# Kernel tuning notes

Measured on AMD Instinct MI355X. Metric: run time of the kernel, lower is better.

The kernel has to match this reference:

```python
import jax, jax.numpy as jnp
import numpy as np

H = 128   # hidden_size
E = 300   # embedding_dim
VOC = 32000
B, TP, TC = 8, 160, 160
D2 = 2 * H  # bidirectional feature dim


def gru_dir(x, Wih, Whh, bih, bhh, reverse):
    # x: [B,T,I] -> hidden states [B,T,Hs]; torch GRU gate order (r,z,n)
    Hs = Whh.shape[1]
    xg = jnp.einsum('bti,gi->btg', x, Wih) + bih  # [B,T,3Hs]
    if reverse:
        xg = xg[:, ::-1]
    def step(h, xt):
        gh = h @ Whh.T + bhh
        xr, xz, xn = jnp.split(xt, 3, axis=-1)
        hr, hz, hn = jnp.split(gh, 3, axis=-1)
        r = jax.nn.sigmoid(xr + hr)
        z = jax.nn.sigmoid(xz + hz)
        n = jnp.tanh(xn + r * hn)
        h = (1.0 - z) * n + z * h
        return h, h
    h0 = jnp.zeros((x.shape[0], Hs), x.dtype)
    _, hs = jax.lax.scan(step, h0, jnp.swapaxes(xg, 0, 1))
    hs = jnp.swapaxes(hs, 0, 1)
    if reverse:
        hs = hs[:, ::-1]
    return hs


def bigru(x, Wf, Uf, bif, bhf, Wb, Ub, bib, bhb):
    return jnp.concatenate([
        gru_dir(x, Wf, Uf, bif, bhf, False),
        gru_dir(x, Wb, Ub, bib, bhb, True)], axis=-1)


def setup_inputs() -> dict:
    key = jax.random.key(0)
    ks = iter(jax.random.split(key, 64))
    def rn(shape, s=0.05):
        return jax.random.normal(next(ks), shape, jnp.float32) * s
    inp = {}
    inp['text_a'] = jax.random.randint(next(ks), (B, TP), 0, VOC)
    inp['text_b'] = jax.random.randint(next(ks), (B, TC), 0, VOC)
    inp['emb'] = rn((VOC, E), 0.1)
    for pfx, ins in [('p', E), ('c', E), ('a', 6 * D2)]:
        for d in ('f', 'b'):
            inp[pfx + '_Wih_' + d] = rn((3 * H, ins))
            inp[pfx + '_Whh_' + d] = rn((3 * H, H))
            inp[pfx + '_bih_' + d] = jnp.zeros((3 * H,), jnp.float32)
            inp[pfx + '_bhh_' + d] = jnp.zeros((3 * H,), jnp.float32)
    inp['Wc1'] = rn((H, D2)); inp['Wc2'] = rn((H, D2)); inp['Vc'] = rn((H,))
    inp['Wb'] = rn((D2, D2))
    inp['Wd'] = rn((H, D2)); inp['Vd'] = rn((H,))
    inp['Wm'] = rn((H, D2)); inp['Vm'] = rn((H,))
    inp['Ws'] = rn((H, D2)); inp['Vs'] = rn((H,))
    inp['Wp'] = rn((H, D2)); inp['Vp'] = rn((H,))
    inp['W1'] = rn((H, D2)); inp['W2'] = rn((H, D2)); inp['Vv'] = rn((H,))
    inp['Wout'] = rn((2, D2)); inp['bout'] = jnp.zeros((2,), jnp.float32)
    return inp


def _forward(text_a, text_b, emb,
             p_Wih_f, p_Whh_f, p_bih_f, p_bhh_f, p_Wih_b, p_Whh_b, p_bih_b, p_bhh_b,
             c_Wih_f, c_Whh_f, c_bih_f, c_bhh_f, c_Wih_b, c_Whh_b, c_bih_b, c_bhh_b,
             a_Wih_f, a_Whh_f, a_bih_f, a_bhh_f, a_Wih_b, a_Whh_b, a_bih_b, a_bhh_b,
             Wc1, Wc2, Vc, Wb, Wd, Vd, Wm, Vm, Ws, Vs, Wp, Vp, W1, W2, Vv, Wout, bout):
    hp = bigru(emb[text_a], p_Wih_f, p_Whh_f, p_bih_f, p_bhh_f,
               p_Wih_b, p_Whh_b, p_bih_b, p_bhh_b)          # [B,Tp,2H]
    hc = bigru(emb[text_b], c_Wih_f, c_Whh_f, c_bih_f, c_bhh_f,
               c_Wih_b, c_Whh_b, c_bih_b, c_bhh_b)          # [B,Tc,2H]
    # concat (additive) attention: [B,Tc,Tp,H]
    s = jnp.tanh((hp @ Wc1.T)[:, None] + (hc @ Wc2.T)[:, :, None])
    a_cat = jax.nn.softmax(s @ Vc, axis=2)                   # [B,Tc,Tp]
    concat_rep = jnp.einsum('bct,btd->bcd', a_cat, hp)
    # bilinear attention
    a_bil = jax.nn.softmax(jnp.einsum('bcd,btd->bct', hc, hp @ Wb.T), axis=2)
    bil_rep = jnp.einsum('bct,btd->bcd', a_bil, hp)
    # dot / minus attention on [B,Tc,Tp,2H] broadcasts
    hp4 = hp[:, None]; hc4 = hc[:, :, None]
    a_dot = jax.nn.softmax(jnp.tanh((hp4 * hc4) @ Wd.T) @ Vd, axis=2)
    dot_rep = jnp.einsum('bct,btd->bcd', a_dot, hp)
    a_min = jax.nn.softmax(jnp.tanh((hp4 - hc4) @ Wm.T) @ Vm, axis=2)
    minus_rep = jnp.einsum('bct,btd->bcd', a_min, hp)
    # self attention on hc: [B,Tc,Tc,2H]
    a_self = jax.nn.softmax(jnp.tanh((hc[:, None] * hc[:, :, None]) @ Ws.T) @ Vs, axis=2)
    self_rep = jnp.einsum('bct,btd->bcd', a_self, hc)
    agg_in = jnp.concatenate([hc, self_rep, concat_rep, dot_rep, bil_rep, minus_rep], axis=-1)
    agg = bigru(agg_in, a_Wih_f, a_Whh_f, a_bih_f, a_bhh_f,
                a_Wih_b, a_Whh_b, a_bih_b, a_bhh_b)          # [B,Tc,2H]
    # pooled passage rep
    ap = jax.nn.softmax(jnp.tanh(hp @ Wp.T) @ Vp, axis=-1)   # [B,Tp]
    rp = jnp.einsum('bt,btd->bd', ap, hp)                    # [B,2H]
    # final attention over aggregation (note: no tanh, faithful to source)
    sc = (agg @ W1.T + (rp @ W2.T)[:, None]) @ Vv            # [B,Tc]
    ac = jax.nn.softmax(sc, axis=-1)
    rc = jnp.einsum('bc,bcd->bd', ac, agg)                   # [B,2H]
    return rc @ Wout.T + bout                                # [B,2] logits


def reference(text_a, text_b, emb,
              p_Wih_f, p_Whh_f, p_bih_f, p_bhh_f, p_Wih_b, p_Whh_b, p_bih_b, p_bhh_b,
              c_Wih_f, c_Whh_f, c_bih_f, c_bhh_f, c_Wih_b, c_Whh_b, c_bih_b, c_bhh_b,
              a_Wih_f, a_Whh_f, a_bih_f, a_bhh_f, a_Wih_b, a_Whh_b, a_bih_b, a_bhh_b,
              Wc1, Wc2, Vc, Wb, Wd, Vd, Wm, Vm, Ws, Vs, Wp, Vp, W1, W2, Vv, Wout, bout):
    return _forward(text_a, text_b, emb,
                    p_Wih_f, p_Whh_f, p_bih_f, p_bhh_f, p_Wih_b, p_Whh_b, p_bih_b, p_bhh_b,
                    c_Wih_f, c_Whh_f, c_bih_f, c_bhh_f, c_Wih_b, c_Whh_b, c_bih_b, c_bhh_b,
                    a_Wih_f, a_Whh_f, a_bih_f, a_bhh_f, a_Wih_b, a_Whh_b, a_bih_b, a_bhh_b,
                    Wc1, Wc2, Vc, Wb, Wd, Vd, Wm, Vm, Ws, Vs, Wp, Vp, W1, W2, Vv, Wout, bout)
```

## Files before the change

### kernel.cpp

```cpp
#include <hip/hip_runtime.h>

#define BB 8
#define TT 160
#define EE 300
#define HH 128
#define D2 256
#define G3 384
#define PSTR 40

typedef __attribute__((ext_vector_type(8))) short bf16x8;
typedef __attribute__((ext_vector_type(4))) float floatx4;

__device__ inline float fsigmoid(float x){ return 1.f/(1.f+__expf(-x)); }
__device__ inline float ftanh(float x){ return 2.f*fsigmoid(2.f*x) - 1.f; }

__device__ inline void split2(float x, unsigned short& hi, unsigned short& lo){
  unsigned ux = __float_as_uint(x);
  hi = (unsigned short)(ux>>16);
  float r = x - __uint_as_float(ux & 0xFFFF0000u);
  lo = (unsigned short)(__float_as_uint(r)>>16);
}

__global__ __launch_bounds__(256) void k_embed(const int* ta, const int* tb,
    const float* emb, float* ep, float* ec){
  const int idx = blockIdx.x*256 + threadIdx.x;
  const int per = BB*TT*EE;
  if (idx < per){
    const int e = idx % EE, bt = idx / EE;
    ep[idx] = emb[(long)ta[bt]*EE + e];
  } else {
    const int j = idx - per;
    const int e = j % EE, bt = j / EE;
    ec[j] = emb[(long)tb[bt]*EE + e];
  }
}

__global__ __launch_bounds__(256) void k_splitarr(const float* a, const float* b, int n,
    unsigned short* ahi, unsigned short* alo, unsigned short* bhi, unsigned short* blo){
  const int idx = blockIdx.x*256 + threadIdx.x;
  if (idx < n){
    split2(a[idx], ahi[idx], alo[idx]);
    split2(b[idx], bhi[idx], blo[idx]);
  }
}

struct GemmJob {
  const float* A; const float* W; const float* bias;
  float* C; int N; int K;
};
struct GemmJobs { GemmJob j[6]; };

__global__ __launch_bounds__(256) void k_gemm(GemmJobs jobs){
  const GemmJob J = jobs.j[blockIdx.z];
  const int tid = threadIdx.x;
  const int lane = tid & 63, w = tid >> 6;
  const int l15 = lane & 15, q = lane >> 4;
  const int n0 = blockIdx.x * 64;
  if (n0 >= J.N) return;
  const int K = J.K;
  const long mrow = blockIdx.y*64 + w*16 + l15;
  const float* Arow = J.A + mrow*K;
  floatx4 acc[4];
  #pragma unroll
  for (int t=0;t<4;t++) acc[t] = (floatx4)0.f;
  const int nch = (K+31)>>5;
  for (int kc=0; kc<nch; kc++){
    const int k0 = kc<<5;
    const int kb = k0 + q*8;
    const bool full = (k0+32 <= K);
    float av[8];
    if (full){
      const floatx4 a0 = *(const floatx4*)(Arow+kb);
      const floatx4 a1 = *(const floatx4*)(Arow+kb+4);
      av[0]=a0[0];av[1]=a0[1];av[2]=a0[2];av[3]=a0[3];
      av[4]=a1[0];av[5]=a1[1];av[6]=a1[2];av[7]=a1[3];
    } else {
      #pragma unroll
      for (int j=0;j<8;j++){ const int k=kb+j; av[j] = (k<K)? Arow[k] : 0.f; }
    }
    union { bf16x8 v; unsigned short u[8]; } ahi, alo;
    #pragma unroll
    for (int j=0;j<8;j++) split2(av[j], ahi.u[j], alo.u[j]);
    #pragma unroll
    for (int t=0;t<4;t++){
      const int n = n0 + t*16 + l15;
      const float* Wr = J.W + (long)n*K + kb;
      float wv[8];
      if (full){
        const floatx4 w0 = *(const floatx4*)(Wr);
        const floatx4 w1 = *(const floatx4*)(Wr+4);
        wv[0]=w0[0];wv[1]=w0[1];wv[2]=w0[2];wv[3]=w0[3];
        wv[4]=w1[0];wv[5]=w1[1];wv[6]=w1[2];wv[7]=w1[3];
      } else {
        #pragma unroll
        for (int j=0;j<8;j++){ const int k=kb+j; wv[j] = (k<K)? Wr[j] : 0.f; }
      }
      union { bf16x8 v; unsigned short u[8]; } whi, wlo;
      #pragma unroll
      for (int j=0;j<8;j++) split2(wv[j], whi.u[j], wlo.u[j]);
      acc[t] = __builtin_amdgcn_mfma_f32_16x16x32_bf16(ahi.v, whi.v, acc[t], 0,0,0);
      acc[t] = __builtin_amdgcn_mfma_f32_16x16x32_bf16(ahi.v, wlo.v, acc[t], 0,0,0);
      acc[t] = __builtin_amdgcn_mfma_f32_16x16x32_bf16(alo.v, whi.v, acc[t], 0,0,0);
    }
  }
  const long rbase = blockIdx.y*64 + w*16 + q*4;
  #pragma unroll
  for (int t=0;t<4;t++){
    const int n = n0 + t*16 + l15;
    const float bv = J.bias ? J.bias[n] : 0.f;
    #pragma unroll
    for (int r=0;r<4;r++)
      J.C[(rbase+r)*(long)J.N + n] = acc[t][r] + bv;
  }
}

struct GruJob { const float* xg; const float* Whh; const float* bhh; float* out; int ocol; int rev; };
struct GruJobs { GruJob j[4]; };

__global__ __launch_bounds__(768) void k_gru(GruJobs jobs){
  const GruJob J = jobs.j[blockIdx.y];
  const int bi = blockIdx.x;
  const int tid = threadIdx.x;
  const int g = tid >> 1, p = tid & 1;
  __shared__ float h_sh[HH];
  __shared__ float gh_sh[G3];
  __shared__ float xt_sh[G3];
  float wr[64];
  {
    const float* wp = J.Whh + (long)g*HH + p*64;
    #pragma unroll
    for (int k=0;k<64;k+=4){
      const floatx4 t4 = *(const floatx4*)(wp+k);
      wr[k]=t4[0]; wr[k+1]=t4[1]; wr[k+2]=t4[2]; wr[k+3]=t4[3];
    }
  }
  const float bhh = J.bhh[g];
  if (tid < HH) h_sh[tid] = 0.f;
  float hreg = 0.f;
  float xv = 0.f;
  {
    const int t0 = J.rev ? (TT-1) : 0;
    if (tid < G3) xv = J.xg[((long)bi*TT + t0)*G3 + tid];
  }
  __syncthreads();
  for (int t=0;t<TT;t++){
    const int tt = J.rev ? (TT-1-t) : t;
    if (tid < G3) xt_sh[tid] = xv;
    if (t+1 < TT){
      const int tn = J.rev ? (TT-2-t) : (t+1);
      if (tid < G3) xv = J.xg[((long)bi*TT + tn)*G3 + tid];
    }
    float gh = 0.f;
    #pragma unroll
    for (int k=0;k<64;k+=4){
      const floatx4 h4 = *(const floatx4*)&h_sh[p*64 + k];
      gh += wr[k]*h4[0] + wr[k+1]*h4[1] + wr[k+2]*h4[2] + wr[k+3]*h4[3];
    }
    gh += __shfl_xor(gh, 1);
    if (p==0) gh_sh[g] = gh + bhh;
    __syncthreads();
    if (tid < HH){
      const float r = fsigmoid(xt_sh[tid]       + gh_sh[tid]);
      const float z = fsigmoid(xt_sh[tid+HH]    + gh_sh[tid+HH]);
      const float n = ftanh  (xt_sh[tid+2*HH]  + r*gh_sh[tid+2*HH]);
      const float h = (1.f-z)*n + z*hreg;
      hreg = h;
      h_sh[tid] = h;
      J.out[((long)bi*TT + tt)*D2 + J.ocol + tid] = h;
    }
    __syncthreads();
  }
}

__device__ inline float block_softmax160(float s, int tid, float* red){
  float m = s;
  #pragma unroll
  for (int o=32;o>0;o>>=1) m = fmaxf(m, __shfl_xor(m,o));
  if ((tid&63)==0) red[tid>>6] = m;
  __syncthreads();
  m = fmaxf(fmaxf(red[0],red[1]), fmaxf(red[2],red[3]));
  const float p = (tid<TT) ? __expf(s-m) : 0.f;
  float t = p;
  #pragma unroll
  for (int o=32;o>0;o>>=1) t += __shfl_xor(t,o);
  if ((tid&63)==0) red[4+(tid>>6)] = t;
  __syncthreads();
  const float sum = red[4]+red[5]+red[6]+red[7];
  return p / sum;
}

__device__ inline float block_softmax160_512(float s, int tid, float* red){
  float m = s;
  #pragma unroll
  for (int o=32;o>0;o>>=1) m = fmaxf(m, __shfl_xor(m,o));
  if ((tid&63)==0) red[tid>>6] = m;
  __syncthreads();
  m = red[0];
  #pragma unroll
  for (int i=1;i<8;i++) m = fmaxf(m, red[i]);
  const float p = (tid<TT) ? __expf(s-m) : 0.f;
  float t = p;
  #pragma unroll
  for (int o=32;o>0;o>>=1) t += __shfl_xor(t,o);
  if ((tid&63)==0) red[8+(tid>>6)] = t;
  __syncthreads();
  float sum = red[8];
  #pragma unroll
  for (int i=1;i<8;i++) sum += red[8+i];
  return p / sum;
}

struct PairJob { const unsigned short* Phi; const unsigned short* Plo;
                 const float* Q; const float* W; const float* V; float* a_out; };

__global__ __launch_bounds__(512) void k_pairattn(PairJob j0, PairJob j1){
  const PairJob J = blockIdx.z ? j1 : j0;
  const int b = blockIdx.y, c = blockIdx.x;
  const int tid = threadIdx.x;
  const int lane = tid & 63, w = tid >> 6;
  const int l15 = lane & 15, q = lane >> 4;
  __shared__ unsigned short Pb[2*2*160*PSTR];
  __shared__ float Qs[D2];
  __shared__ float sc_sh[TT];
  __shared__ float red[16];
  if (tid < D2) Qs[tid] = J.Q[((long)b*TT + c)*D2 + tid];
  if (tid < TT) sc_sh[tid] = 0.f;
  const long pbase = (long)b*TT*D2;

  int s_hl[5], s_t[5], s_d4[5];
  #pragma unroll
  for (int r=0;r<5;r++){
    const int idx = tid + r*512;
    const int hl = (idx >= 1280) ? 1 : 0;
    const int e4 = idx - hl*1280;
    s_hl[r] = hl; s_t[r] = e4 >> 3; s_d4[r] = e4 & 7;
  }
  uint2 stg[5];
  #pragma unroll
  for (int r=0;r<5;r++){
    const unsigned short* src = (s_hl[r] ? J.Plo : J.Phi) + pbase + (long)s_t[r]*D2 + 0*32 + s_d4[r]*4;
    stg[r] = *(const uint2*)src;
  }
  const float* Wbase = J.W + (long)(w*16 + l15)*D2;
  floatx4 wv0 = *(const floatx4*)(Wbase + q*8);
  floatx4 wv1 = *(const floatx4*)(Wbase + q*8 + 4);
  #pragma unroll
  for (int r=0;r<5;r++)
    *(uint2*)&Pb[((0*2 + s_hl[r])*160 + s_t[r])*PSTR + s_d4[r]*4] = stg[r];
  __syncthreads();

  floatx4 acc[10];
  #pragma unroll
  for (int nt=0;nt<10;nt++) acc[nt] = (floatx4)0.f;

  for (int kc=0; kc<8; kc++){
    const floatx4 wc0 = wv0, wc1 = wv1;
    if (kc < 7){
      wv0 = *(const floatx4*)(Wbase + (kc+1)*32 + q*8);
      wv1 = *(const floatx4*)(Wbase + (kc+1)*32 + q*8 + 4);
      #pragma unroll
      for (int r=0;r<5;r++){
        const unsigned short* src = (s_hl[r] ? J.Plo : J.Phi) + pbase + (long)s_t[r]*D2 + (kc+1)*32 + s_d4[r]*4;
        stg[r] = *(const uint2*)src;
      }
    }
    const int d0 = kc*32 + q*8;
    const floatx4 q0 = *(const floatx4*)&Qs[d0];
    const floatx4 q1 = *(const floatx4*)&Qs[d0+4];
    union { bf16x8 v; unsigned short u[8]; } ah, al;
    #pragma unroll
    for (int j=0;j<4;j++){
      split2(wc0[j]*q0[j], ah.u[j],   al.u[j]);
      split2(wc1[j]*q1[j], ah.u[4+j], al.u[4+j]);
    }
    const int buf = kc & 1;
    #pragma unroll
    for (int nt=0;nt<10;nt++){
      const int t = nt*16 + l15;
      union { bf16x8 v; } bh, bl;
      bh.v = *(const bf16x8*)&Pb[((buf*2+0)*160 + t)*PSTR + q*8];
      bl.v = *(const bf16x8*)&Pb[((buf*2+1)*160 + t)*PSTR + q*8];
      acc[nt] = __builtin_amdgcn_mfma_f32_16x16x32_bf16(ah.v, bh.v, acc[nt], 0,0,0);
      acc[nt] = __builtin_amdgcn_mfma_f32_16x16x32_bf16(ah.v, bl.v, acc[nt], 0,0,0);
      acc[nt] = __builtin_amdgcn_mfma_f32_16x16x32_bf16(al.v, bh.v, acc[nt], 0,0,0);
    }
    if (kc < 7){
      const int nbuf = 1 - buf;
      #pragma unroll
      for (int r=0;r<5;r++)
        *(uint2*)&Pb[((nbuf*2 + s_hl[r])*160 + s_t[r])*PSTR + s_d4[r]*4] = stg[r];
      __syncthreads();
    }
  }

  float vreg[4];
  #pragma unroll
  for (int r=0;r<4;r++) vreg[r] = J.V[w*16 + q*4 + r];
  #pragma unroll
  for (int nt=0;nt<10;nt++){
    float pp = 0.f;
    #pragma unroll
    for (int r=0;r<4;r++) pp += vreg[r]*ftanh(acc[nt][r]);
    pp += __shfl_xor(pp,16);
    pp += __shfl_xor(pp,32);
    if (q==0) atomicAdd(&sc_sh[nt*16 + l15], pp);
  }
  __syncthreads();
  const float s = (tid<TT)? sc_sh[tid] : -INFINITY;
  const float a = block_softmax160_512(s, tid, red);
  if (tid < TT) J.a_out[((long)b*TT + c)*TT + tid] = a;
}

struct AddJob { const float* up; const float* uc; const float* V; float sgn; float* a_out; };

__global__ __launch_bounds__(256) void k_addattn(AddJob j0, AddJob j1){
  const AddJob J = blockIdx.z ? j1 : j0;
  const int b = blockIdx.y, c = blockIdx.x, tid = threadIdx.x;
  __shared__ float ucc[HH];
  __shared__ float vv[HH];
  __shared__ float red[8];
  if (tid < HH){
    ucc[tid] = J.sgn * J.uc[((long)b*TT + c)*HH + tid];
    vv[tid] = J.V[tid];
  }
  __syncthreads();
  float s = -INFINITY;
  if (tid < TT){
    const float* ur = J.up + ((long)b*TT + tid)*HH;
    float a0 = 0.f;
    #pragma unroll 4
    for (int k=0;k<HH;k++) a0 += vv[k]*ftanh(ur[k]+ucc[k]);
    s = a0;
  }
  const float a = block_softmax160(s, tid, red);
  if (tid < TT) J.a_out[((long)b*TT + c)*TT + tid] = a;
}

__global__ __launch_bounds__(256) void k_bilattn(const float* hc, const float* hpWb, float* a_out){
  const int b = blockIdx.y, c = blockIdx.x, tid = threadIdx.x;
  __shared__ float hcc[D2];
  __shared__ float red[8];
  if (tid < D2) hcc[tid] = hc[((long)b*TT + c)*D2 + tid];
  __syncthreads();
  float s = -INFINITY;
  if (tid < TT){
    const float* pr = hpWb + ((long)b*TT + tid)*D2;
    float a0 = 0.f;
    #pragma unroll 4
    for (int k=0;k<D2;k++) a0 += hcc[k]*pr[k];
    s = a0;
  }
  const float a = block_softmax160(s, tid, red);
  if (tid < TT) a_out[((long)b*TT + c)*TT + tid] = a;
}

__global__ __launch_bounds__(256) void k_rep(const float* hp, const float* hc,
    const float* acat, const float* abil, const float* adot, const float* amin, const float* aself,
    float* aggin){
  const int b = blockIdx.y, c = blockIdx.x, tid = threadIdx.x;
  __shared__ float a5[5][TT];
  {
    const long base = ((long)b*TT + c)*TT;
    for (int i=tid;i<5*TT;i+=256){
      const int which = i/TT, t = i - which*TT;
      const float* p = which==0? acat : which==1? abil : which==2? adot : which==3? amin : aself;
      a5[which][t] = p[base + t];
    }
  }
  __syncthreads();
  const float* hpb = hp + (long)b*TT*D2 + tid;
  const float* hcb = hc + (long)b*TT*D2 + tid;
  float r0=0.f,r1=0.f,r2=0.f,r3=0.f,r4=0.f;
  for (int t=0;t<TT;t++){
    const float vp = hpb[(long)t*D2];
    const float vc = hcb[(long)t*D2];
    r0 += a5[0][t]*vp;
    r1 += a5[1][t]*vp;
    r2 += a5[2][t]*vp;
    r3 += a5[3][t]*vp;
    r4 += a5[4][t]*vc;
  }
  float* o = aggin + ((long)b*TT + c)*(6*D2);
  o[tid]        = hc[((long)b*TT + c)*D2 + tid];
  o[D2 + tid]   = r4;
  o[2*D2 + tid] = r0;
  o[3*D2 + tid] = r2;
  o[4*D2 + tid] = r1;
  o[5*D2 + tid] = r3;
}

__global__ __launch_bounds__(256) void k_tail1(const float* upP, const float* Vp,
    const float* hp, float* rp){
  const int b = blockIdx.x, tid = threadIdx.x;
  __shared__ float vv[HH];
  __shared__ float ap_sh[TT];
  __shared__ float red[8];
  if (tid<HH) vv[tid] = Vp[tid];
  __syncthreads();
  float s = -INFINITY;
  if (tid<TT){
    const float* ur = upP + ((long)b*TT + tid)*HH;
    float a0=0.f;
    #pragma unroll 4
    for (int k=0;k<HH;k++) a0 += vv[k]*ftanh(ur[k]);
    s = a0;
  }
  const float a = block_softmax160(s, tid, red);
  if (tid<TT) ap_sh[tid] = a;
  __syncthreads();
  float acc = 0.f;
  const float* hpb = hp + (long)b*TT*D2 + tid;
  for (int t=0;t<TT;t++) acc += ap_sh[t]*hpb[(long)t*D2];
  rp[b*D2 + tid] = acc;
}

__global__ __launch_bounds__(256) void k_tail2(const float* aggW1, const float* agg, const float* rp,
    const float* W2, const float* Vv, const float* Wout, const float* bout,
    float* out){
  const int b = blockIdx.x, tid = threadIdx.x;
  __shared__ float rpw[HH];
  __shared__ float ac_sh[TT];
  __shared__ float rc_sh[D2];
  __shared__ float red[8];
  if (tid < HH){
    float a0=0.f;
    const float* wr2 = W2 + (long)tid*D2;
    const float* rr = rp + b*D2;
    for (int d=0; d<D2; d++) a0 += wr2[d]*rr[d];
    rpw[tid] = a0;
  }
  __syncthreads();
  float s = -INFINITY;
  if (tid < TT){
    const float* ar = aggW1 + ((long)b*TT + tid)*HH;
    float a0=0.f;
    for (int k=0;k<HH;k++) a0 += Vv[k]*(ar[k] + rpw[k]);
    s = a0;
  }
  const float a = block_softmax160(s, tid, red);
  if (tid < TT) ac_sh[tid] = a;
  __syncthreads();
  float rc=0.f;
  const float* ab = agg + (long)b*TT*D2 + tid;
  for (int t=0;t<TT;t++) rc += ac_sh[t]*ab[(long)t*D2];
  rc_sh[tid] = rc;
  __syncthreads();
  if (tid < 2){
    float o = bout[tid];
    const float* wr = Wout + (long)tid*D2;
    for (int d=0; d<D2; d++) o += wr[d]*rc_sh[d];
    out[b*2 + tid] = o;
  }
}

extern "C" void kernel_launch(void* const* d_in, const int* in_sizes, int n_in,
                              void* d_out, int out_size, void* d_ws, size_t ws_size,
                              hipStream_t stream){
  (void)in_sizes; (void)n_in; (void)out_size; (void)ws_size;
  const int* ta = (const int*)d_in[0];
  const int* tb = (const int*)d_in[1];
  const float* emb = (const float*)d_in[2];
  #define F32(i) ((const float*)d_in[i])

  float* ws = (float*)d_ws;
  float* ep    = ws;
  float* ec    = ep    + 384000;
  float* xg_pf = ec    + 384000;
  float* xg_pb = xg_pf + 491520;
  float* xg_cf = xg_pb + 491520;
  float* xg_cb = xg_cf + 491520;
  float* hp    = xg_cb + 491520;
  float* hc    = hp    + 327680;
  float* up1   = hc    + 327680;
  float* uc2   = up1   + 163840;
  float* ump   = uc2   + 163840;
  float* umc   = ump   + 163840;
  float* upP   = umc   + 163840;
  float* hpWb  = upP   + 163840;
  float* acat  = hpWb  + 327680;
  float* abil  = acat  + 204800;
  float* adot  = abil  + 204800;
  float* amin  = adot  + 204800;
  float* aself = amin  + 204800;
  float* aggin = aself + 204800;
  float* rp    = aggin + 1966080;
  unsigned short* hp_hi = (unsigned short*)(rp + 2048);
  unsigned short* hp_lo = hp_hi + 327680;
  unsigned short* hc_hi = hp_lo + 327680;
  unsigned short* hc_lo = hc_hi + 327680;
  float* xg_af = xg_pf;
  float* xg_ab = xg_pb;
  float* agg   = xg_cf;
  float* aggW1 = xg_cb;

  k_embed<<<dim3(3000), dim3(256), 0, stream>>>(ta, tb, emb, ep, ec);

  GemmJobs ja = {};
  ja.j[0] = {ep, F32(3),  F32(5),  xg_pf, 384, 300};
  ja.j[1] = {ep, F32(7),  F32(9),  xg_pb, 384, 300};
  ja.j[2] = {ec, F32(11), F32(13), xg_cf, 384, 300};
  ja.j[3] = {ec, F32(15), F32(17), xg_cb, 384, 300};
  k_gemm<<<dim3(6,20,4), dim3(256), 0, stream>>>(ja);

  GruJobs gj = {};
  gj.j[0] = {xg_pf, F32(4),  F32(6),  hp, 0,   0};
  gj.j[1] = {xg_pb, F32(8),  F32(10), hp, 128, 1};
  gj.j[2] = {xg_cf, F32(12), F32(14), hc, 0,   0};
  gj.j[3] = {xg_cb, F32(16), F32(18), hc, 128, 1};
  k_gru<<<dim3(8,4), dim3(768), 0, stream>>>(gj);

  k_splitarr<<<dim3(1280), dim3(256), 0, stream>>>(hp, hc, 327680, hp_hi, hp_lo, hc_hi, hc_lo);

  GemmJobs jb = {};
  jb.j[0] = {hp, F32(27), nullptr, up1,  128, 256};
  jb.j[1] = {hc, F32(28), nullptr, uc2,  128, 256};
  jb.j[2] = {hp, F32(33), nullptr, ump,  128, 256};
  jb.j[3] = {hc, F32(33), nullptr, umc,  128, 256};
  jb.j[4] = {hp, F32(37), nullptr, upP,  128, 256};
  jb.j[5] = {hp, F32(30), nullptr, hpWb, 256, 256};
  k_gemm<<<dim3(4,20,6), dim3(256), 0, stream>>>(jb);

  PairJob pd  = {hp_hi, hp_lo, hc, F32(31), F32(32), adot};
  PairJob psf = {hc_hi, hc_lo, hc, F32(35), F32(36), aself};
  k_pairattn<<<dim3(160,8,2), dim3(512), 0, stream>>>(pd, psf);

  AddJob ac_ = {up1, uc2, F32(29),  1.f, acat};
  AddJob am_ = {ump, umc, F32(34), -1.f, amin};
  k_addattn<<<dim3(160,8,2), dim3(256), 0, stream>>>(ac_, am_);

  k_bilattn<<<dim3(160,8), dim3(256), 0, stream>>>(hc, hpWb, abil);

  k_tail1<<<dim3(8), dim3(256), 0, stream>>>(upP, F32(38), hp, rp);

  k_rep<<<dim3(160,8), dim3(256), 0, stream>>>(hp, hc, acat, abil, adot, amin, aself, aggin);

  GemmJobs jc = {};
  jc.j[0] = {aggin, F32(19), F32(21), xg_af, 384, 1536};
  jc.j[1] = {aggin, F32(23), F32(25), xg_ab, 384, 1536};
  k_gemm<<<dim3(6,20,2), dim3(256), 0, stream>>>(jc);

  GruJobs gja = {};
  gja.j[0] = {xg_af, F32(20), F32(22), agg, 0,   0};
  gja.j[1] = {xg_ab, F32(24), F32(26), agg, 128, 1};
  k_gru<<<dim3(8,2), dim3(768), 0, stream>>>(gja);

  GemmJobs jd = {};
  jd.j[0] = {agg, F32(39), nullptr, aggW1, 128, 256};
  k_gemm<<<dim3(2,20,1), dim3(256), 0, stream>>>(jd);

  k_tail2<<<dim3(8), dim3(256), 0, stream>>>(aggW1, agg, rp, F32(40), F32(41), F32(42), F32(43),
                                             (float*)d_out);
  #undef F32
}
```

Before: 927.5 us.

## Compute GRU recurrent matvec with split-bf16 MFMA and double-buffered hidden state

The recurrent h·Whh^T product in the GRU kernel now runs on bf16 MFMA instructions, using a hi/lo split of both weights and hidden state so results stay close to fp32. Weights are pre-split into registers, and 8 waves each own 16 rows of every gate. The hidden state is double-buffered in shared memory, so only one barrier per timestep is needed instead of two. Each gate update now runs in the lanes that own the accumulator rows. The cost is extra MFMA work, since only one column of the 16-wide B operand is used, plus per-step split overhead and a small precision change.

```diff
diff --git a/kernel.cpp b/kernel.cpp
--- a/kernel.cpp
+++ b/kernel.cpp
@@ -117,56 +117,102 @@
 struct GruJob { const float* xg; const float* Whh; const float* bhh; float* out; int ocol; int rev; };
 struct GruJobs { GruJob j[4]; };
 
-__global__ __launch_bounds__(768) void k_gru(GruJobs jobs){
+__global__ __launch_bounds__(512) void k_gru(GruJobs jobs){
   const GruJob J = jobs.j[blockIdx.y];
   const int bi = blockIdx.x;
   const int tid = threadIdx.x;
-  const int g = tid >> 1, p = tid & 1;
-  __shared__ float h_sh[HH];
-  __shared__ float gh_sh[G3];
-  __shared__ float xt_sh[G3];
-  float wr[64];
-  {
-    const float* wp = J.Whh + (long)g*HH + p*64;
-    #pragma unroll
-    for (int k=0;k<64;k+=4){
-      const floatx4 t4 = *(const floatx4*)(wp+k);
-      wr[k]=t4[0]; wr[k+1]=t4[1]; wr[k+2]=t4[2]; wr[k+3]=t4[3];
-    }
-  }
-  const float bhh = J.bhh[g];
-  if (tid < HH) h_sh[tid] = 0.f;
-  float hreg = 0.f;
-  float xv = 0.f;
+  const int lane = tid & 63, w = tid >> 6;
+  const int l15 = lane & 15, q = lane >> 4;
+  const bool act = (l15 == 0);
+  __shared__ float h_sh[2][132];
+
+  union BF { bf16x8 v; unsigned short u[8]; };
+  BF Ah[3][4], Al[3][4];
+  #pragma unroll
+  for (int it=0; it<3; it++){
+    const float* wr = J.Whh + (long)((it*8 + w)*16 + l15)*HH;
+    #pragma unroll
+    for (int kc=0; kc<4; kc++){
+      const floatx4 w0 = *(const floatx4*)(wr + kc*32 + q*8);
+      const floatx4 w1 = *(const floatx4*)(wr + kc*32 + q*8 + 4);
+      #pragma unroll
+      for (int jj=0; jj<4; jj++){
+        split2(w0[jj], Ah[it][kc].u[jj],   Al[it][kc].u[jj]);
+        split2(w1[jj], Ah[it][kc].u[4+jj], Al[it][kc].u[4+jj]);
+      }
+    }
+  }
+  const int j0 = w*16 + q*4;
+  floatx4 bhr = *(const floatx4*)(J.bhh + j0);
+  floatx4 bhz = *(const floatx4*)(J.bhh + 128 + j0);
+  floatx4 bhn = *(const floatx4*)(J.bhh + 256 + j0);
+  floatx4 hreg = (floatx4)0.f;
+
+  for (int i = tid; i < 2*132; i += 512) ((float*)h_sh)[i] = 0.f;
+
+  floatx4 xr=(floatx4)0.f, xz=(floatx4)0.f, xn=(floatx4)0.f;
   {
     const int t0 = J.rev ? (TT-1) : 0;
-    if (tid < G3) xv = J.xg[((long)bi*TT + t0)*G3 + tid];
-  }
-  __syncthreads();
-  for (int t=0;t<TT;t++){
+    if (act){
+      const float* xgp = J.xg + ((long)bi*TT + t0)*G3;
+      xr = *(const floatx4*)(xgp + j0);
+      xz = *(const floatx4*)(xgp + 128 + j0);
+      xn = *(const floatx4*)(xgp + 256 + j0);
+    }
+  }
+  __syncthreads();
+
+  for (int t=0; t<TT; t++){
     const int tt = J.rev ? (TT-1-t) : t;
-    if (tid < G3) xt_sh[tid] = xv;
-    if (t+1 < TT){
+    const int buf = t & 1;
+    const floatx4 cxr=xr, cxz=xz, cxn=xn;
+    if (act && t+1 < TT){
       const int tn = J.rev ? (TT-2-t) : (t+1);
-      if (tid < G3) xv = J.xg[((long)bi*TT + tn)*G3 + tid];
-    }
-    float gh = 0.f;
-    #pragma unroll
-    for (int k=0;k<64;k+=4){
-      const floatx4 h4 = *(const floatx4*)&h_sh[p*64 + k];
-      gh += wr[k]*h4[0] + wr[k+1]*h4[1] + wr[k+2]*h4[2] + wr[k+3]*h4[3];
-    }
-    gh += __shfl_xor(gh, 1);
-    if (p==0) gh_sh[g] = gh + bhh;
-    __syncthreads();
-    if (tid < HH){
-      const float r = fsigmoid(xt_sh[tid]       + gh_sh[tid]);
-      const float z = fsigmoid(xt_sh[tid+HH]    + gh_sh[tid+HH]);
-      const float n = ftanh  (xt_sh[tid+2*HH]  + r*gh_sh[tid+2*HH]);
-      const float h = (1.f-z)*n + z*hreg;
-      hreg = h;
-      h_sh[tid] = h;
-      J.out[((long)bi*TT + tt)*D2 + J.ocol + tid] = h;
+      const float* xgp = J.xg + ((long)bi*TT + tn)*G3;
+      xr = *(const floatx4*)(xgp + j0);
+      xz = *(const floatx4*)(xgp + 128 + j0);
+      xn = *(const floatx4*)(xgp + 256 + j0);
+    }
+    floatx4 accr=(floatx4)0.f, accz=(floatx4)0.f, accn=(floatx4)0.f;
+    #pragma unroll
+    for (int kc=0; kc<4; kc++){
+      BF Bh2, Bl2;
+      if (act){
+        const float* hp8 = &h_sh[buf][kc*32 + q*8];
+        const floatx4 h0 = *(const floatx4*)hp8;
+        const floatx4 h1 = *(const floatx4*)(hp8+4);
+        #pragma unroll
+        for (int jj=0; jj<4; jj++){
+          split2(h0[jj], Bh2.u[jj],   Bl2.u[jj]);
+          split2(h1[jj], Bh2.u[4+jj], Bl2.u[4+jj]);
+        }
+      } else {
+        #pragma unroll
+        for (int jj=0; jj<8; jj++){ Bh2.u[jj]=0; Bl2.u[jj]=0; }
+      }
+      accr = __builtin_amdgcn_mfma_f32_16x16x32_bf16(Ah[0][kc].v, Bh2.v, accr, 0,0,0);
+      accz = __builtin_amdgcn_mfma_f32_16x16x32_bf16(Ah[1][kc].v, Bh2.v, accz, 0,0,0);
+      accn = __builtin_amdgcn_mfma_f32_16x16x32_bf16(Ah[2][kc].v, Bh2.v, accn, 0,0,0);
+      accr = __builtin_amdgcn_mfma_f32_16x16x32_bf16(Ah[0][kc].v, Bl2.v, accr, 0,0,0);
+      accz = __builtin_amdgcn_mfma_f32_16x16x32_bf16(Ah[1][kc].v, Bl2.v, accz, 0,0,0);
+      accn = __builtin_amdgcn_mfma_f32_16x16x32_bf16(Ah[2][kc].v, Bl2.v, accn, 0,0,0);
+      accr = __builtin_amdgcn_mfma_f32_16x16x32_bf16(Al[0][kc].v, Bh2.v, accr, 0,0,0);
+      accz = __builtin_amdgcn_mfma_f32_16x16x32_bf16(Al[1][kc].v, Bh2.v, accz, 0,0,0);
+      accn = __builtin_amdgcn_mfma_f32_16x16x32_bf16(Al[2][kc].v, Bh2.v, accn, 0,0,0);
+    }
+    const int nbuf = 1 - buf;
+    if (act){
+      floatx4 hnew;
+      #pragma unroll
+      for (int r=0; r<4; r++){
+        const float gr = fsigmoid(cxr[r] + accr[r] + bhr[r]);
+        const float gz = fsigmoid(cxz[r] + accz[r] + bhz[r]);
+        const float gn = ftanh  (cxn[r] + gr*(accn[r] + bhn[r]));
+        hnew[r] = (1.f-gz)*gn + gz*hreg[r];
+      }
+      hreg = hnew;
+      *(floatx4*)&h_sh[nbuf][j0] = hnew;
+      *(floatx4*)(J.out + ((long)bi*TT + tt)*D2 + J.ocol + j0) = hnew;
     }
     __syncthreads();
   }
@@ -507,7 +553,7 @@
   gj.j[1] = {xg_pb, F32(8),  F32(10), hp, 128, 1};
   gj.j[2] = {xg_cf, F32(12), F32(14), hc, 0,   0};
   gj.j[3] = {xg_cb, F32(16), F32(18), hc, 128, 1};
-  k_gru<<<dim3(8,4), dim3(768), 0, stream>>>(gj);
+  k_gru<<<dim3(8,4), dim3(512), 0, stream>>>(gj);
 
   k_splitarr<<<dim3(1280), dim3(256), 0, stream>>>(hp, hc, 327680, hp_hi, hp_lo, hc_hi, hc_lo);
 
@@ -542,7 +588,7 @@
   GruJobs gja = {};
   gja.j[0] = {xg_af, F32(20), F32(22), agg, 0,   0};
   gja.j[1] = {xg_ab, F32(24), F32(26), agg, 128, 1};
-  k_gru<<<dim3(8,2), dim3(768), 0, stream>>>(gja);
+  k_gru<<<dim3(8,2), dim3(512), 0, stream>>>(gja);
 
   GemmJobs jd = {};
   jd.j[0] = {agg, F32(39), nullptr, aggW1, 128, 256};
```

New measurement: 1.532 ms. 1.65x slower.

## Pre-split GEMM weights once and shrink GRU block to fuse gate math

Applied to the files above, without the earlier changes.

A new kernel converts every GEMM weight matrix into bf16 hi/lo halves (padded in K) once per call, so the GEMM kernels load the split values instead of re-splitting fp32 weights in every tile. The GRU kernel moves from 768 to 256 threads: each thread pair keeps all three gate rows of Whh in registers, computes the r/z/n dot products together, and applies the gate nonlinearities in the same threads, using a double-buffered hidden state. This removes the gh/xt shared-memory round trip and one barrier per timestep from the serial recurrence. The cost is an extra weight-split launch plus scratch memory, and 192 weight registers per thread in the GRU, which risks spilling.

```diff
diff --git a/kernel.cpp b/kernel.cpp
--- a/kernel.cpp
+++ b/kernel.cpp
@@ -44,20 +44,32 @@
   }
 }
 
-struct GemmJob {
-  const float* A; const float* W; const float* bias;
-  float* C; int N; int K;
+struct SplitJob { const float* W; unsigned short* hi; unsigned short* lo; int n; int K; int Kp; };
+struct SplitJobs { SplitJob j[12]; };
+
+__global__ __launch_bounds__(256) void k_splitw(SplitJobs jobs){
+  const SplitJob J = jobs.j[blockIdx.z];
+  const int idx = blockIdx.x*256 + threadIdx.x;
+  if (idx >= J.n) return;
+  const int row = idx / J.Kp, k = idx - row*J.Kp;
+  const float v = (k < J.K) ? J.W[(long)row*J.K + k] : 0.f;
+  split2(v, J.hi[idx], J.lo[idx]);
+}
+
+struct GemmSJob {
+  const float* A; const unsigned short* Whi; const unsigned short* Wlo; const float* bias;
+  float* C; int N; int K; int Kp;
 };
-struct GemmJobs { GemmJob j[6]; };
-
-__global__ __launch_bounds__(256) void k_gemm(GemmJobs jobs){
-  const GemmJob J = jobs.j[blockIdx.z];
+struct GemmSJobs { GemmSJob j[6]; };
+
+__global__ __launch_bounds__(256) void k_gemmS(GemmSJobs jobs){
+  const GemmSJob J = jobs.j[blockIdx.z];
   const int tid = threadIdx.x;
   const int lane = tid & 63, w = tid >> 6;
   const int l15 = lane & 15, q = lane >> 4;
   const int n0 = blockIdx.x * 64;
   if (n0 >= J.N) return;
-  const int K = J.K;
+  const int K = J.K, Kp = J.Kp;
   const long mrow = blockIdx.y*64 + w*16 + l15;
   const float* Arow = J.A + mrow*K;
   floatx4 acc[4];
@@ -67,9 +79,8 @@
   for (int kc=0; kc<nch; kc++){
     const int k0 = kc<<5;
     const int kb = k0 + q*8;
-    const bool full = (k0+32 <= K);
     float av[8];
-    if (full){
+    if (k0+32 <= K){
       const floatx4 a0 = *(const floatx4*)(Arow+kb);
       const floatx4 a1 = *(const floatx4*)(Arow+kb+4);
       av[0]=a0[0];av[1]=a0[1];av[2]=a0[2];av[3]=a0[3];
@@ -84,20 +95,10 @@
     #pragma unroll
     for (int t=0;t<4;t++){
       const int n = n0 + t*16 + l15;
-      const float* Wr = J.W + (long)n*K + kb;
-      float wv[8];
-      if (full){
-        const floatx4 w0 = *(const floatx4*)(Wr);
-        const floatx4 w1 = *(const floatx4*)(Wr+4);
-        wv[0]=w0[0];wv[1]=w0[1];wv[2]=w0[2];wv[3]=w0[3];
-        wv[4]=w1[0];wv[5]=w1[1];wv[6]=w1[2];wv[7]=w1[3];
-      } else {
-        #pragma unroll
-        for (int j=0;j<8;j++){ const int k=kb+j; wv[j] = (k<K)? Wr[j] : 0.f; }
-      }
-      union { bf16x8 v; unsigned short u[8]; } whi, wlo;
-      #pragma unroll
-      for (int j=0;j<8;j++) split2(wv[j], whi.u[j], wlo.u[j]);
+      const long wo = (long)n*Kp + kb;
+      union { bf16x8 v; uint4 d; } whi, wlo;
+      whi.d = *(const uint4*)(J.Whi + wo);
+      wlo.d = *(const uint4*)(J.Wlo + wo);
       acc[t] = __builtin_amdgcn_mfma_f32_16x16x32_bf16(ahi.v, whi.v, acc[t], 0,0,0);
       acc[t] = __builtin_amdgcn_mfma_f32_16x16x32_bf16(ahi.v, wlo.v, acc[t], 0,0,0);
       acc[t] = __builtin_amdgcn_mfma_f32_16x16x32_bf16(alo.v, whi.v, acc[t], 0,0,0);
@@ -117,56 +118,67 @@
 struct GruJob { const float* xg; const float* Whh; const float* bhh; float* out; int ocol; int rev; };
 struct GruJobs { GruJob j[4]; };
 
-__global__ __launch_bounds__(768) void k_gru(GruJobs jobs){
+__global__ __launch_bounds__(256,1) void k_gru(GruJobs jobs){
   const GruJob J = jobs.j[blockIdx.y];
   const int bi = blockIdx.x;
   const int tid = threadIdx.x;
-  const int g = tid >> 1, p = tid & 1;
-  __shared__ float h_sh[HH];
-  __shared__ float gh_sh[G3];
-  __shared__ float xt_sh[G3];
-  float wr[64];
+  const int j = tid >> 1, p = tid & 1;
+  __shared__ float h_sh[2][HH];
+  float wr[64], wz[64], wn[64];
   {
-    const float* wp = J.Whh + (long)g*HH + p*64;
+    const float* r0 = J.Whh + (long)j*HH + p*64;
+    const float* z0 = J.Whh + (long)(HH+j)*HH + p*64;
+    const float* n0 = J.Whh + (long)(2*HH+j)*HH + p*64;
     #pragma unroll
     for (int k=0;k<64;k+=4){
-      const floatx4 t4 = *(const floatx4*)(wp+k);
-      wr[k]=t4[0]; wr[k+1]=t4[1]; wr[k+2]=t4[2]; wr[k+3]=t4[3];
-    }
-  }
-  const float bhh = J.bhh[g];
-  if (tid < HH) h_sh[tid] = 0.f;
+      *(floatx4*)&wr[k] = *(const floatx4*)(r0+k);
+      *(floatx4*)&wz[k] = *(const floatx4*)(z0+k);
+      *(floatx4*)&wn[k] = *(const floatx4*)(n0+k);
+    }
+  }
+  float bhr=0.f,bhz=0.f,bhn=0.f, xr=0.f,xz=0.f,xn=0.f;
+  if (p==0){
+    bhr = J.bhh[j]; bhz = J.bhh[HH+j]; bhn = J.bhh[2*HH+j];
+    const int t0 = J.rev ? (TT-1) : 0;
+    const float* xgp = J.xg + ((long)bi*TT + t0)*G3;
+    xr = xgp[j]; xz = xgp[HH+j]; xn = xgp[2*HH+j];
+  }
+  ((float*)h_sh)[tid] = 0.f;
   float hreg = 0.f;
-  float xv = 0.f;
-  {
-    const int t0 = J.rev ? (TT-1) : 0;
-    if (tid < G3) xv = J.xg[((long)bi*TT + t0)*G3 + tid];
-  }
   __syncthreads();
   for (int t=0;t<TT;t++){
     const int tt = J.rev ? (TT-1-t) : t;
-    if (tid < G3) xt_sh[tid] = xv;
-    if (t+1 < TT){
+    const int buf = t & 1;
+    const float cxr=xr, cxz=xz, cxn=xn;
+    if (p==0 && t+1 < TT){
       const int tn = J.rev ? (TT-2-t) : (t+1);
-      if (tid < G3) xv = J.xg[((long)bi*TT + tn)*G3 + tid];
-    }
-    float gh = 0.f;
-    #pragma unroll
-    for (int k=0;k<64;k+=4){
-      const floatx4 h4 = *(const floatx4*)&h_sh[p*64 + k];
-      gh += wr[k]*h4[0] + wr[k+1]*h4[1] + wr[k+2]*h4[2] + wr[k+3]*h4[3];
-    }
-    gh += __shfl_xor(gh, 1);
-    if (p==0) gh_sh[g] = gh + bhh;
-    __syncthreads();
-    if (tid < HH){
-      const float r = fsigmoid(xt_sh[tid]       + gh_sh[tid]);
-      const float z = fsigmoid(xt_sh[tid+HH]    + gh_sh[tid+HH]);
-      const float n = ftanh  (xt_sh[tid+2*HH]  + r*gh_sh[tid+2*HH]);
-      const float h = (1.f-z)*n + z*hreg;
+      const float* xgp = J.xg + ((long)bi*TT + tn)*G3;
+      xr = xgp[j]; xz = xgp[HH+j]; xn = xgp[2*HH+j];
+    }
+    float ar0=0.f,ar1=0.f, az0=0.f,az1=0.f, an0=0.f,an1=0.f;
+    #pragma unroll
+    for (int k=0;k<64;k+=8){
+      const floatx4 h0 = *(const floatx4*)&h_sh[buf][p*64+k];
+      const floatx4 h1 = *(const floatx4*)&h_sh[buf][p*64+k+4];
+      ar0 += wr[k]*h0[0] + wr[k+1]*h0[1] + wr[k+2]*h0[2] + wr[k+3]*h0[3];
+      az0 += wz[k]*h0[0] + wz[k+1]*h0[1] + wz[k+2]*h0[2] + wz[k+3]*h0[3];
+      an0 += wn[k]*h0[0] + wn[k+1]*h0[1] + wn[k+2]*h0[2] + wn[k+3]*h0[3];
+      ar1 += wr[k+4]*h1[0] + wr[k+5]*h1[1] + wr[k+6]*h1[2] + wr[k+7]*h1[3];
+      az1 += wz[k+4]*h1[0] + wz[k+5]*h1[1] + wz[k+6]*h1[2] + wz[k+7]*h1[3];
+      an1 += wn[k+4]*h1[0] + wn[k+5]*h1[1] + wn[k+6]*h1[2] + wn[k+7]*h1[3];
+    }
+    float ar = ar0+ar1, az = az0+az1, an = an0+an1;
+    ar += __shfl_xor(ar,1);
+    az += __shfl_xor(az,1);
+    an += __shfl_xor(an,1);
+    if (p==0){
+      const float gr = fsigmoid(cxr + ar + bhr);
+      const float gz = fsigmoid(cxz + az + bhz);
+      const float gn = ftanh  (cxn + gr*(an + bhn));
+      const float h = (1.f-gz)*gn + gz*hreg;
       hreg = h;
-      h_sh[tid] = h;
-      J.out[((long)bi*TT + tt)*D2 + J.ocol + tid] = h;
+      h_sh[1-buf][j] = h;
+      J.out[((long)bi*TT + tt)*D2 + J.ocol + j] = h;
     }
     __syncthreads();
   }
@@ -238,7 +250,7 @@
   uint2 stg[5];
   #pragma unroll
   for (int r=0;r<5;r++){
-    const unsigned short* src = (s_hl[r] ? J.Plo : J.Phi) + pbase + (long)s_t[r]*D2 + 0*32 + s_d4[r]*4;
+    const unsigned short* src = (s_hl[r] ? J.Plo : J.Phi) + pbase + (long)s_t[r]*D2 + s_d4[r]*4;
     stg[r] = *(const uint2*)src;
   }
   const float* Wbase = J.W + (long)(w*16 + l15)*D2;
@@ -488,37 +500,64 @@
   unsigned short* hp_lo = hp_hi + 327680;
   unsigned short* hc_hi = hp_lo + 327680;
   unsigned short* hc_lo = hc_hi + 327680;
+  unsigned short* wsp = hc_lo + 327680;
+  unsigned short* w3h  = wsp;             unsigned short* w3l  = w3h  + 122880;
+  unsigned short* w7h  = w3l  + 122880;   unsigned short* w7l  = w7h  + 122880;
+  unsigned short* w11h = w7l  + 122880;   unsigned short* w11l = w11h + 122880;
+  unsigned short* w15h = w11l + 122880;   unsigned short* w15l = w15h + 122880;
+  unsigned short* w27h = w15l + 122880;   unsigned short* w27l = w27h + 32768;
+  unsigned short* w28h = w27l + 32768;    unsigned short* w28l = w28h + 32768;
+  unsigned short* w33h = w28l + 32768;    unsigned short* w33l = w33h + 32768;
+  unsigned short* w37h = w33l + 32768;    unsigned short* w37l = w37h + 32768;
+  unsigned short* w30h = w37l + 32768;    unsigned short* w30l = w30h + 65536;
+  unsigned short* w19h = w30l + 65536;    unsigned short* w19l = w19h + 589824;
+  unsigned short* w23h = w19l + 589824;   unsigned short* w23l = w23h + 589824;
+  unsigned short* w39h = w23l + 589824;   unsigned short* w39l = w39h + 32768;
   float* xg_af = xg_pf;
   float* xg_ab = xg_pb;
   float* agg   = xg_cf;
   float* aggW1 = xg_cb;
 
   k_embed<<<dim3(3000), dim3(256), 0, stream>>>(ta, tb, emb, ep, ec);
-
-  GemmJobs ja = {};
-  ja.j[0] = {ep, F32(3),  F32(5),  xg_pf, 384, 300};
-  ja.j[1] = {ep, F32(7),  F32(9),  xg_pb, 384, 300};
-  ja.j[2] = {ec, F32(11), F32(13), xg_cf, 384, 300};
-  ja.j[3] = {ec, F32(15), F32(17), xg_cb, 384, 300};
-  k_gemm<<<dim3(6,20,4), dim3(256), 0, stream>>>(ja);
+  SplitJobs sj = {};
+  sj.j[0]  = {F32(3),  w3h,  w3l,  122880, 300, 320};
+  sj.j[1]  = {F32(7),  w7h,  w7l,  122880, 300, 320};
+  sj.j[2]  = {F32(11), w11h, w11l, 122880, 300, 320};
+  sj.j[3]  = {F32(15), w15h, w15l, 122880, 300, 320};
+  sj.j[4]  = {F32(27), w27h, w27l, 32768,  256, 256};
+  sj.j[5]  = {F32(28), w28h, w28l, 32768,  256, 256};
+  sj.j[6]  = {F32(33), w33h, w33l, 32768,  256, 256};
+  sj.j[7]  = {F32(37), w37h, w37l, 32768,  256, 256};
+  sj.j[8]  = {F32(30), w30h, w30l, 65536,  256, 256};
+  sj.j[9]  = {F32(19), w19h, w19l, 589824, 1536, 1536};
+  sj.j[10] = {F32(23), w23h, w23l, 589824, 1536, 1536};
+  sj.j[11] = {F32(39), w39h, w39l, 32768,  256, 256};
+  k_splitw<<<dim3(2304,1,12), dim3(256), 0, stream>>>(sj);
+
+  GemmSJobs ja = {};
+  ja.j[0] = {ep, w3h,  w3l,  F32(5),  xg_pf, 384, 300, 320};
+  ja.j[1] = {ep, w7h,  w7l,  F32(9),  xg_pb, 384, 300, 320};
+  ja.j[2] = {ec, w11h, w11l, F32(13), xg_cf, 384, 300, 320};
+  ja.j[3] = {ec, w15h, w15l, F32(17), xg_cb, 384, 300, 320};
+  k_gemmS<<<dim3(6,20,4), dim3(256), 0, stream>>>(ja);
 
   GruJobs gj = {};
   gj.j[0] = {xg_pf, F32(4),  F32(6),  hp, 0,   0};
   gj.j[1] = {xg_pb, F32(8),  F32(10), hp, 128, 1};
   gj.j[2] = {xg_cf, F32(12), F32(14), hc, 0,   0};
   gj.j[3] = {xg_cb, F32(16), F32(18), hc, 128, 1};
-  k_gru<<<dim3(8,4), dim3(768), 0, stream>>>(gj);
+  k_gru<<<dim3(8,4), dim3(256), 0, stream>>>(gj);
 
   k_splitarr<<<dim3(1280), dim3(256), 0, stream>>>(hp, hc, 327680, hp_hi, hp_lo, hc_hi, hc_lo);
 
-  GemmJobs jb = {};
-  jb.j[0] = {hp, F32(27), nullptr, up1,  128, 256};
-  jb.j[1] = {hc, F32(28), nullptr, uc2,  128, 256};
-  jb.j[2] = {hp, F32(33), nullptr, ump,  128, 256};
-  jb.j[3] = {hc, F32(33), nullptr, umc,  128, 256};
-  jb.j[4] = {hp, F32(37), nullptr, upP,  128, 256};
-  jb.j[5] = {hp, F32(30), nullptr, hpWb, 256, 256};
-  k_gemm<<<dim3(4,20,6), dim3(256), 0, stream>>>(jb);
+  GemmSJobs jb = {};
+  jb.j[0] = {hp, w27h, w27l, nullptr, up1,  128, 256, 256};
+  jb.j[1] = {hc, w28h, w28l, nullptr, uc2,  128, 256, 256};
+  jb.j[2] = {hp, w33h, w33l, nullptr, ump,  128, 256, 256};
+  jb.j[3] = {hc, w33h, w33l, nullptr, umc,  128, 256, 256};
+  jb.j[4] = {hp, w37h, w37l, nullptr, upP,  128, 256, 256};
+  jb.j[5] = {hp, w30h, w30l, nullptr, hpWb, 256, 256, 256};
+  k_gemmS<<<dim3(4,20,6), dim3(256), 0, stream>>>(jb);
 
   PairJob pd  = {hp_hi, hp_lo, hc, F32(31), F32(32), adot};
   PairJob psf = {hc_hi, hc_lo, hc, F32(35), F32(36), aself};
@@ -534,19 +573,19 @@
 
   k_rep<<<dim3(160,8), dim3(256), 0, stream>>>(hp, hc, acat, abil, adot, amin, aself, aggin);
 
-  GemmJobs jc = {};
-  jc.j[0] = {aggin, F32(19), F32(21), xg_af, 384, 1536};
-  jc.j[1] = {aggin, F32(23), F32(25), xg_ab, 384, 1536};
-  k_gemm<<<dim3(6,20,2), dim3(256), 0, stream>>>(jc);
+  GemmSJobs jc = {};
+  jc.j[0] = {aggin, w19h, w19l, F32(21), xg_af, 384, 1536, 1536};
+  jc.j[1] = {aggin, w23h, w23l, F32(25), xg_ab, 384, 1536, 1536};
+  k_gemmS<<<dim3(6,20,2), dim3(256), 0, stream>>>(jc);
 
   GruJobs gja = {};
   gja.j[0] = {xg_af, F32(20), F32(22), agg, 0,   0};
   gja.j[1] = {xg_ab, F32(24), F32(26), agg, 128, 1};
-  k_gru<<<dim3(8,2), dim3(768), 0, stream>>>(gja);
-
-  GemmJobs jd = {};
-  jd.j[0] = {agg, F32(39), nullptr, aggW1, 128, 256};
-  k_gemm<<<dim3(2,20,1), dim3(256), 0, stream>>>(jd);
+  k_gru<<<dim3(8,2), dim3(256), 0, stream>>>(gja);
+
+  GemmSJobs jd = {};
+  jd.j[0] = {agg, w39h, w39l, nullptr, aggW1, 128, 256, 256};
+  k_gemmS<<<dim3(2,20,1), dim3(256), 0, stream>>>(jd);
 
   k_tail2<<<dim3(8), dim3(256), 0, stream>>>(aggW1, agg, rp, F32(40), F32(41), F32(42), F32(43),
                                              (float*)d_out);
```

Result: faster. 868.1 us (-6.4%).
